# Kernel optimization log

Measured on AMD Instinct MI355X. Metric: run time of the kernel, lower is better.

## Reference

```python
import jax, jax.numpy as jnp
import numpy as np

N, I, R, A, O, HEADS, HW, KS = 16, 128, 256, 256, 256, 8, 24, 3
HC = A // HEADS  # head channels
DN = ('NCHW', 'OIHW', 'NCHW')


def _conv(x, w, padding):
    return jax.lax.conv_general_dilated(x, w, (1, 1), padding, dimension_numbers=DN)


def setup_inputs() -> dict:
    key = jax.random.key(0)
    ks = jax.random.split(key, 16)
    g = lambda k, shape, fan: jax.random.normal(k, shape, jnp.float32) * (fan ** -0.5)
    return {
        'x': jax.random.normal(ks[0], (N, I, HW, HW), jnp.float32),
        'h0': jax.random.normal(ks[1], (N, R, HW, HW), jnp.float32) * 0.1,
        'c0': jax.random.normal(ks[2], (N, R, HW, HW), jnp.float32) * 0.1,
        'w_in': g(ks[3], (R, I, 1, 1), I),
        'b_in': jnp.zeros((R,), jnp.float32),
        'wq_x': g(ks[4], (A, R, KS, KS), R * KS * KS * 2 * HC),
        'wq_h': g(ks[5], (A, R, KS, KS), R * KS * KS * 2 * HC),
        'wk_x': g(ks[6], (A, R, KS, KS), R * KS * KS),
        'wk_h': g(ks[7], (A, R, KS, KS), R * KS * KS),
        'wv_x': g(ks[8], (A, R, KS, KS), R * KS * KS * 2),
        'wv_h': g(ks[9], (A, R, KS, KS), R * KS * KS * 2),
        'bv': jnp.zeros((A,), jnp.float32),
        'wg_a': g(ks[10], (4 * R, A, 1, 1), A * 3),
        'bg': jnp.zeros((4 * R,), jnp.float32),
        'wg_x': g(ks[11], (4 * R, R, KS, KS), R * KS * KS * 3),
        'wg_h': g(ks[12], (4 * R, R, KS, KS), R * KS * KS * 3),
        'w_out': g(ks[13], (O, R, 1, 1), R),
        'b_out': jnp.zeros((O,), jnp.float32),
    }


def reference(x, h0, c0, w_in, b_in, wq_x, wq_h, wk_x, wk_h, wv_x, wv_h, bv,
              wg_a, bg, wg_x, wg_h, w_out, b_out):
    # input accumulation (1x1 conv per input, summed; single input here)
    xin = _conv(x, w_in, 'VALID') + b_in[None, :, None, None]  # [N,R,H,W]
    # q: SAME-padded 3x3 convs of x and h (Accumulate = sum)
    q = _conv(xin, wq_x, 'SAME') + _conv(h0, wq_h, 'SAME')      # [N,A,H,W]
    # k, v: VALID 3x3 convs -> spatially reduced key/value positions
    k = _conv(xin, wk_x, 'VALID') + _conv(h0, wk_h, 'VALID')    # [N,A,H-2,W-2]
    v = _conv(xin, wv_x, 'VALID') + _conv(h0, wv_h, 'VALID') + bv[None, :, None, None]
    Q = HW * HW
    D = (HW - KS + 1) * (HW - KS + 1)
    qh = q.reshape(N, HEADS, HC, Q)
    kh = k.reshape(N, HEADS, HC, D)
    vh = v.reshape(N, HEADS, HC, D)
    w = jax.nn.softmax(jnp.einsum('ngcq,ngcd->ngqd', qh, kh), axis=-1)  # [N,G,Q,D]
    a = jnp.einsum('ngcd,ngqd->ngcq', vh, w).reshape(N, A, HW, HW)
    # fused i,f,g,o gate projections: 1x1 conv on a + 3x3 SAME convs on x and h
    gates = (_conv(a, wg_a, 'VALID') + bg[None, :, None, None]
             + _conv(xin, wg_x, 'SAME') + _conv(h0, wg_h, 'SAME'))      # [N,4R,H,W]
    i, f, gg, o = jnp.split(gates, 4, axis=1)
    c = jax.nn.sigmoid(f) * c0 + jax.nn.sigmoid(i) * jnp.tanh(gg)
    h = jax.nn.sigmoid(o) * jnp.tanh(c)
    return _conv(h, w_out, 'VALID') + b_out[None, :, None, None]
```

## Files before the change

### kernel.cpp

```cpp
#include <hip/hip_runtime.h>
#include <cstddef>

constexpr int kN  = 16;
constexpr int kI  = 128;
constexpr int kHW = 24;
constexpr int kQ  = 576;
constexpr int kD  = 484;
constexpr int kDP = 512;
constexpr int kPP = 676;

constexpr int kKTQKV = 144;
constexpr int kKTG   = 152;
constexpr int kKTO   = 8;

constexpr size_t H_XPAD   = 0;
constexpr size_t H_HPAD   = 2768896;
constexpr size_t H_APQKV  = 5537792;
constexpr size_t H_APG    = 9076736;
constexpr size_t H_APO    = 14057472;
constexpr size_t H_A16    = 14123008;
constexpr size_t H_H16    = 16482304;
constexpr size_t H_Q16C   = 18841600;
constexpr size_t H_KT16   = 21200896;
constexpr size_t H_VC16   = 23298048;

using half8    = __attribute__((ext_vector_type(8))) _Float16;
using floatx16 = __attribute__((ext_vector_type(16))) float;

__device__ __forceinline__ float sigm(float x) { return 1.0f / (1.0f + __expf(-x)); }
__device__ __forceinline__ float tanh_f(float x) {
    float e = __expf(2.0f * fabsf(x));
    float r = 1.0f - 2.0f / (e + 1.0f);
    return copysignf(r, x);
}
__device__ __forceinline__ half8 LD8(const _Float16* p) { return *(const half8*)p; }
__device__ __forceinline__ void ST8(_Float16* p, half8 v) { *(half8*)p = v; }


__global__ void pack_qkv_kernel(const float* __restrict__ wq_x, const float* __restrict__ wq_h,
                                const float* __restrict__ wk_x, const float* __restrict__ wk_h,
                                const float* __restrict__ wv_x, const float* __restrict__ wv_h,
                                _Float16* __restrict__ dst) {
    int pidx = blockIdx.x * 256 + threadIdx.x;
    int j = pidx & 7, row = (pidx >> 3) & 255, hl = (pidx >> 11) & 1, kk = (pidx >> 12) & 1;
    int tile = pidx >> 13;
    int mb = tile / kKTQKV, kt = tile - mb * kKTQKV;
    int k = kt * 32 + kk * 16 + hl * 8 + j;
    int srcs = (k >= 2304) ? 1 : 0;
    int r = k - srcs * 2304;
    int tap = r >> 8, ic = r & 255;
    const float* w;
    if (mb == 0)      w = srcs ? wq_h : wq_x;
    else if (mb == 1) w = srcs ? wk_h : wk_x;
    else              w = srcs ? wv_h : wv_x;
    dst[pidx] = (_Float16)w[((size_t)row * 256 + ic) * 9 + tap];
}

__global__ void pack_gates_kernel(const float* __restrict__ wg_x, const float* __restrict__ wg_h,
                                  const float* __restrict__ wg_a, _Float16* __restrict__ dst) {
    int pidx = blockIdx.x * 256 + threadIdx.x;
    int j = pidx & 7, row = (pidx >> 3) & 255, hl = (pidx >> 11) & 1, kk = (pidx >> 12) & 1;
    int tile = pidx >> 13;
    int mb = tile / kKTG, kt = tile - mb * kKTG;
    int P = mb * 256 + row;
    int T = P >> 5, ch_local = (P >> 2) & 7, g = P & 3;
    int m = g * 256 + T * 8 + ch_local;
    int k = kt * 32 + kk * 16 + hl * 8 + j;
    float val;
    if (k < 4608) {
        int srcs = (k >= 2304) ? 1 : 0;
        int r = k - srcs * 2304;
        int tap = r >> 8, ic = r & 255;
        const float* w = srcs ? wg_h : wg_x;
        val = w[((size_t)m * 256 + ic) * 9 + tap];
    } else {
        val = wg_a[(size_t)m * 256 + (k - 4608)];
    }
    dst[pidx] = (_Float16)val;
}

__global__ void pack_out_kernel(const float* __restrict__ src, _Float16* __restrict__ dst) {
    int pidx = blockIdx.x * 256 + threadIdx.x;
    int j = pidx & 7, row = (pidx >> 3) & 255, hl = (pidx >> 11) & 1, kk = (pidx >> 12) & 1;
    int kt = pidx >> 13;
    int k = kt * 32 + kk * 16 + hl * 8 + j;
    dst[pidx] = (_Float16)src[(size_t)row * 256 + k];
}

__global__ void pad_nhwc_kernel(const float* __restrict__ src, _Float16* __restrict__ dst) {
    __shared__ float tile[32][65];
    int pxt = blockIdx.x, ict = blockIdx.y, n = blockIdx.z;
    int tid = threadIdx.x;
    {
        int icl = tid >> 6, pxl = tid & 63;
        #pragma unroll
        for (int rep = 0; rep < 8; ++rep) {
            int ic = ict * 32 + rep * 4 + icl;
            tile[rep * 4 + icl][pxl] = src[((size_t)n * 256 + ic) * kQ + pxt * 64 + pxl];
        }
    }
    __syncthreads();
    {
        int icl = tid & 31, pxl0 = tid >> 5;
        #pragma unroll
        for (int rep = 0; rep < 8; ++rep) {
            int pxl = rep * 8 + pxl0;
            int px = pxt * 64 + pxl;
            int y = px / kHW, x = px - y * kHW;
            dst[((size_t)n * kPP + (size_t)(y + 1) * 26 + (x + 1)) * 256 + ict * 32 + icl] =
                (_Float16)tile[icl][pxl];
        }
    }
}

__global__ void conv1x1_pad_kernel(const float* __restrict__ x, const float* __restrict__ w,
                                   const float* __restrict__ b, _Float16* __restrict__ out) {
    int px = blockIdx.x * 64 + threadIdx.x;
    int n = blockIdx.z;
    int oc0 = __builtin_amdgcn_readfirstlane(blockIdx.y * 16 + threadIdx.y * 4);
    const float* ip = x + (size_t)n * kI * kQ + px;
    float acc[4] = {0.f, 0.f, 0.f, 0.f};
    #pragma unroll 4
    for (int ic = 0; ic < kI; ++ic) {
        float xv = ip[(size_t)ic * kQ];
        #pragma unroll
        for (int j = 0; j < 4; ++j) acc[j] = fmaf(xv, w[(size_t)(oc0 + j) * kI + ic], acc[j]);
    }
    int y = px / kHW, xc = px - y * kHW;
    _Float16* op = out + ((size_t)n * kPP + (size_t)(y + 1) * 26 + (xc + 1)) * 256 + oc0;
    #pragma unroll
    for (int j = 0; j < 4; ++j) op[j] = (_Float16)(acc[j] + b[oc0 + j]);
}

template<int BMODE, int EMODE>
__global__ __launch_bounds__(256)
void gemm_kernel(const _Float16* __restrict__ Apack,
                 const _Float16* __restrict__ B1, const _Float16* __restrict__ B2,
                 const _Float16* __restrict__ B3,
                 _Float16* __restrict__ q16, _Float16* __restrict__ k16,
                 _Float16* __restrict__ v16, _Float16* __restrict__ h16,
                 const float* __restrict__ c0, float* __restrict__ outf,
                 const float* __restrict__ bias, int Ktiles, int Ktot) {
    __shared__ _Float16 Bs[2][2048];
    const int tid = threadIdx.x;
    const int wv = tid >> 6, lane = tid & 63, l31 = lane & 31, hl = lane >> 5;
    const int nt = blockIdx.x, mb = blockIdx.y, n = blockIdx.z;

    floatx16 acc00 = {}, acc01 = {}, acc10 = {}, acc11 = {};

    const _Float16* aK0 = Apack + (size_t)mb * Ktiles * 8192
                        + hl * 2048 + (size_t)(wv * 64 + l31) * 8;
    const _Float16* aK1 = aK0 + 4096;

    const int px_l = tid >> 2, bc = tid & 3;
    const int px = nt * 64 + px_l;
    const int by = px / kHW, bx = px - by * kHW;
    const int wofs = px_l * 32 + ((bc ^ (px_l & 3)) << 3);
    const int sw = l31 & 3;
    const int r00 = l31 * 32 + ((hl ^ sw) << 3);
    const int r10 = l31 * 32 + (((2 + hl) ^ sw) << 3);

    for (int kt = 0; kt < Ktiles; ++kt) {
        const _Float16* bp;
        if (BMODE == 2 && kt >= 144) {
            bp = B3 + ((size_t)n * kQ + px) * 256 + (kt - 144) * 32 + bc * 8;
        } else if (BMODE == 0 || BMODE == 2) {
            int srcs = (kt >= 72) ? 1 : 0;
            int t2 = kt - srcs * 72;
            int tap = t2 >> 3, ict = t2 & 7;
            int ty = (tap * 11) >> 5;
            int tx = tap - ty * 3;
            const _Float16* img = srcs ? B2 : B1;
            bp = img + ((size_t)n * kPP + (size_t)(by + ty) * 26 + (bx + tx)) * 256
                     + ict * 32 + bc * 8;
        } else {
            bp = B1 + ((size_t)n * kQ + px) * Ktot + kt * 32 + bc * 8;
        }
        half8 bv  = LD8(bp);
        half8 a00 = LD8(aK0);
        half8 a0m = LD8(aK0 + 256);
        half8 a10 = LD8(aK1);
        half8 a1m = LD8(aK1 + 256);
        aK0 += 8192; aK1 += 8192;
        ST8(&Bs[kt & 1][wofs], bv);
        __syncthreads();
        const _Float16* bb = Bs[kt & 1];
        half8 b00 = LD8(bb + r00);
        half8 b01 = LD8(bb + r00 + 1024);
        half8 b10 = LD8(bb + r10);
        half8 b11 = LD8(bb + r10 + 1024);
        acc00 = __builtin_amdgcn_mfma_f32_32x32x16_f16(a00, b00, acc00, 0, 0, 0);
        acc01 = __builtin_amdgcn_mfma_f32_32x32x16_f16(a00, b01, acc01, 0, 0, 0);
        acc10 = __builtin_amdgcn_mfma_f32_32x32x16_f16(a0m, b00, acc10, 0, 0, 0);
        acc11 = __builtin_amdgcn_mfma_f32_32x32x16_f16(a0m, b01, acc11, 0, 0, 0);
        acc00 = __builtin_amdgcn_mfma_f32_32x32x16_f16(a10, b10, acc00, 0, 0, 0);
        acc01 = __builtin_amdgcn_mfma_f32_32x32x16_f16(a10, b11, acc01, 0, 0, 0);
        acc10 = __builtin_amdgcn_mfma_f32_32x32x16_f16(a1m, b10, acc10, 0, 0, 0);
        acc11 = __builtin_amdgcn_mfma_f32_32x32x16_f16(a1m, b11, acc11, 0, 0, 0);
    }

    #pragma unroll
    for (int mtile = 0; mtile < 2; ++mtile) {
        #pragma unroll
        for (int ntile = 0; ntile < 2; ++ntile) {
            const floatx16& A = mtile ? (ntile ? acc11 : acc10) : (ntile ? acc01 : acc00);
            const int pxe = nt * 64 + ntile * 32 + l31;
            if (EMODE == 0) {
                const int mrow = wv * 64 + mtile * 32;
                if (mb == 0) {
                    #pragma unroll
                    for (int r = 0; r < 16; ++r) {
                        int rowi = (r & 3) + 8 * (r >> 2) + 4 * hl;
                        q16[((size_t)n * 256 + mrow + rowi) * kQ + pxe] = (_Float16)A[r];
                    }
                } else {
                    int yy = pxe / kHW, xx = pxe - yy * kHW;
                    if (yy >= 1 && yy <= 22 && xx >= 1 && xx <= 22) {
                        int d = (yy - 1) * 22 + (xx - 1);
                        #pragma unroll
                        for (int r = 0; r < 16; ++r) {
                            int ch = mrow + (r & 3) + 8 * (r >> 2) + 4 * hl;
                            int head = n * 8 + (ch >> 5);
                            if (mb == 1)
                                k16[((size_t)head * kDP + d) * 32 + (ch & 31)] = (_Float16)A[r];
                            else
                                v16[((size_t)head * 32 + (ch & 31)) * kDP + d] =
                                    (_Float16)(A[r] + bias[ch]);
                        }
                    }
                }
            } else if (EMODE == 3) {
                const int T = mb * 8 + wv * 2 + mtile;
                #pragma unroll
                for (int q4 = 0; q4 < 4; ++q4) {
                    int c = T * 8 + 2 * q4 + hl;
                    float iv = A[4 * q4 + 0] + bias[c];
                    float fv = A[4 * q4 + 1] + bias[256 + c];
                    float gv = A[4 * q4 + 2] + bias[512 + c];
                    float ov = A[4 * q4 + 3] + bias[768 + c];
                    float c0v = c0[((size_t)n * 256 + c) * kQ + pxe];
                    float cn = sigm(fv) * c0v + sigm(iv) * tanh_f(gv);
                    h16[((size_t)n * kQ + pxe) * 256 + c] = (_Float16)(sigm(ov) * tanh_f(cn));
                }
            } else {
                const int mrow = wv * 64 + mtile * 32;
                #pragma unroll
                for (int r = 0; r < 16; ++r) {
                    int m = mrow + (r & 3) + 8 * (r >> 2) + 4 * hl;
                    outf[((size_t)n * 256 + m) * kQ + pxe] = A[r] + bias[m];
                }
            }
        }
    }
}

__global__ __launch_bounds__(128)
void attn_kernel(const _Float16* __restrict__ q16c, const _Float16* __restrict__ kT16,
                 const _Float16* __restrict__ vC16, _Float16* __restrict__ a16) {
    const int lane = threadIdx.x & 63;
    const int wv   = threadIdx.x >> 6;
    const int l31 = lane & 31, hl = lane >> 5;
    const int head = blockIdx.y;
    const int n = head >> 3, hd = head & 7;
    const int qt = blockIdx.x * 2 + wv;
    const int q0 = qt * 32;

    half8 qf0, qf1;
    {
        const _Float16* qb = q16c + ((size_t)n * 256 + hd * 32 + hl * 8) * kQ + q0 + l31;
        #pragma unroll
        for (int j = 0; j < 8; ++j) {
            qf0[j] = qb[(size_t)j * kQ];
            qf1[j] = qb[(size_t)(16 + j) * kQ];
        }
    }

    const _Float16* kbase0 = kT16 + ((size_t)head * kDP + l31) * 32 + hl * 8;
    const _Float16* vbase0 = vC16 + ((size_t)head * 32 + l31) * kDP + hl * 8;

    floatx16 acc = {};
    float m_run = -1e30f, l_run = 0.f;

    half8 kf0 = LD8(kbase0);
    half8 kf1 = LD8(kbase0 + 16);

    for (int dt = 0; dt < 16; ++dt) {
        const int d0 = dt * 32;
        floatx16 S = {};
        S = __builtin_amdgcn_mfma_f32_32x32x16_f16(kf0, qf0, S, 0, 0, 0);
        S = __builtin_amdgcn_mfma_f32_32x32x16_f16(kf1, qf1, S, 0, 0, 0);

        half8 vf0 = LD8(vbase0 + d0);
        half8 vf1 = LD8(vbase0 + d0 + 16);
        if (dt < 15) {
            kf0 = LD8(kbase0 + (size_t)(d0 + 32) * 32);
            kf1 = LD8(kbase0 + (size_t)(d0 + 32) * 32 + 16);
        }

        if (dt == 15) {
            #pragma unroll
            for (int r = 0; r < 16; ++r)
                if (!(hl == 0 && r < 4)) S[r] = -1e30f;
        }

        float tmax = S[0];
        #pragma unroll
        for (int r = 1; r < 16; ++r) tmax = fmaxf(tmax, S[r]);
        tmax = fmaxf(tmax, __shfl_xor(tmax, 32));
        float mnew = fmaxf(m_run, tmax);
        float f = __expf(m_run - mnew);
        float p[16], psum = 0.f;
        #pragma unroll
        for (int r = 0; r < 16; ++r) { p[r] = __expf(S[r] - mnew); psum += p[r]; }
        psum += __shfl_xor(psum, 32);
        l_run = f * l_run + psum;
        #pragma unroll
        for (int r = 0; r < 16; ++r) acc[r] *= f;
        m_run = mnew;

        float other[16];
        #pragma unroll
        for (int r = 0; r < 16; ++r) other[r] = __shfl_xor(p[r], 32);
        half8 pf0, pf1;
        #pragma unroll
        for (int t = 0; t < 4; ++t) {
            pf0[t]     = (_Float16)(hl ? other[4 + t]  : p[t]);
            pf0[4 + t] = (_Float16)(hl ? p[4 + t]      : other[t]);
            pf1[t]     = (_Float16)(hl ? other[12 + t] : p[8 + t]);
            pf1[4 + t] = (_Float16)(hl ? p[12 + t]     : other[8 + t]);
        }

        acc = __builtin_amdgcn_mfma_f32_32x32x16_f16(vf0, pf0, acc, 0, 0, 0);
        acc = __builtin_amdgcn_mfma_f32_32x32x16_f16(vf1, pf1, acc, 0, 0, 0);
    }

    float inv = 1.f / l_run;
    _Float16* ap = a16 + ((size_t)n * kQ + q0 + l31) * 256 + hd * 32;
    #pragma unroll
    for (int r = 0; r < 16; ++r) {
        int c = (r & 3) + 8 * (r >> 2) + 4 * hl;
        ap[c] = (_Float16)(acc[r] * inv);
    }
}

extern "C" void kernel_launch(void* const* d_in, const int* in_sizes, int n_in,
                              void* d_out, int out_size, void* d_ws, size_t ws_size,
                              hipStream_t stream) {
    (void)in_sizes; (void)n_in; (void)out_size; (void)ws_size;
    const float* x     = (const float*)d_in[0];
    const float* h0    = (const float*)d_in[1];
    const float* c0    = (const float*)d_in[2];
    const float* w_in  = (const float*)d_in[3];
    const float* b_in  = (const float*)d_in[4];
    const float* wq_x  = (const float*)d_in[5];
    const float* wq_h  = (const float*)d_in[6];
    const float* wk_x  = (const float*)d_in[7];
    const float* wk_h  = (const float*)d_in[8];
    const float* wv_x  = (const float*)d_in[9];
    const float* wv_h  = (const float*)d_in[10];
    const float* bv    = (const float*)d_in[11];
    const float* wg_a  = (const float*)d_in[12];
    const float* bg    = (const float*)d_in[13];
    const float* wg_x  = (const float*)d_in[14];
    const float* wg_h  = (const float*)d_in[15];
    const float* w_out = (const float*)d_in[16];
    const float* b_out = (const float*)d_in[17];

    _Float16* wh = (_Float16*)d_ws;
    _Float16* xpad16  = wh + H_XPAD;
    _Float16* hpad16  = wh + H_HPAD;
    _Float16* apqkv   = wh + H_APQKV;
    _Float16* apg     = wh + H_APG;
    _Float16* apo     = wh + H_APO;
    _Float16* a16     = wh + H_A16;
    _Float16* h16     = wh + H_H16;
    _Float16* q16c    = wh + H_Q16C;
    _Float16* kT16    = wh + H_KT16;
    _Float16* vC16    = wh + H_VC16;

    hipMemsetAsync(wh, 0, 11075584, stream);

    pack_qkv_kernel<<<13824, 256, 0, stream>>>(wq_x, wq_h, wk_x, wk_h, wv_x, wv_h, apqkv);
    pack_gates_kernel<<<19456, 256, 0, stream>>>(wg_x, wg_h, wg_a, apg);
    pack_out_kernel<<<256, 256, 0, stream>>>(w_out, apo);

    pad_nhwc_kernel<<<dim3(9, 8, kN), 256, 0, stream>>>(h0, hpad16);
    conv1x1_pad_kernel<<<dim3(9, 16, kN), dim3(64, 4), 0, stream>>>(x, w_in, b_in, xpad16);

    gemm_kernel<0, 0><<<dim3(9, 3, kN), 256, 0, stream>>>(
        apqkv, xpad16, hpad16, nullptr, q16c, kT16, vC16, nullptr,
        nullptr, nullptr, bv, kKTQKV, 0);

    attn_kernel<<<dim3(9, 128), 128, 0, stream>>>(q16c, kT16, vC16, a16);

    gemm_kernel<2, 3><<<dim3(9, 4, kN), 256, 0, stream>>>(
        apg, xpad16, hpad16, a16, nullptr, nullptr, nullptr, h16,
        c0, nullptr, bg, kKTG, 0);

    gemm_kernel<1, 2><<<dim3(9, 1, kN), 256, 0, stream>>>(
        apo, h16, nullptr, nullptr, nullptr, nullptr, nullptr, nullptr,
        nullptr, (float*)d_out, b_out, kKTO, 256);
}
```

Baseline: 526.2 us.

## Halve GEMM M-tile to 128 rows and pad LDS rows instead of XOR swizzle

The GEMM block tile shrinks from 256x64 to 128x64, so each wave now computes one 32-row M-tile with two accumulators instead of four. The grid doubles along M, and the weight pack kernels are reorganised to a 128-row tile layout. The LDS B tile now uses a padded row stride of 40 halves in place of the XOR swizzle, and a second barrier is added per K step. The intent is to launch more blocks for better occupancy and CU coverage. The cost is halved A/B reuse per block, twice as many B loads from global memory, and extra synchronisation.

```diff
diff --git a/kernel.cpp b/kernel.cpp
--- a/kernel.cpp
+++ b/kernel.cpp
@@ -42,27 +42,28 @@
                                 const float* __restrict__ wv_x, const float* __restrict__ wv_h,
                                 _Float16* __restrict__ dst) {
     int pidx = blockIdx.x * 256 + threadIdx.x;
-    int j = pidx & 7, row = (pidx >> 3) & 255, hl = (pidx >> 11) & 1, kk = (pidx >> 12) & 1;
-    int tile = pidx >> 13;
-    int mb = tile / kKTQKV, kt = tile - mb * kKTQKV;
+    int j = pidx & 7, row = (pidx >> 3) & 127, hl = (pidx >> 10) & 1, kk = (pidx >> 11) & 1;
+    int tile = pidx >> 12;
+    int mt = tile / kKTQKV, kt = tile - mt * kKTQKV;
+    int m = mt * 128 + row;
     int k = kt * 32 + kk * 16 + hl * 8 + j;
     int srcs = (k >= 2304) ? 1 : 0;
     int r = k - srcs * 2304;
     int tap = r >> 8, ic = r & 255;
-    const float* w;
-    if (mb == 0)      w = srcs ? wq_h : wq_x;
-    else if (mb == 1) w = srcs ? wk_h : wk_x;
-    else              w = srcs ? wv_h : wv_x;
-    dst[pidx] = (_Float16)w[((size_t)row * 256 + ic) * 9 + tap];
+    const float* w; int mm;
+    if (m < 256)      { w = srcs ? wq_h : wq_x; mm = m; }
+    else if (m < 512) { w = srcs ? wk_h : wk_x; mm = m - 256; }
+    else              { w = srcs ? wv_h : wv_x; mm = m - 512; }
+    dst[pidx] = (_Float16)w[((size_t)mm * 256 + ic) * 9 + tap];
 }
 
 __global__ void pack_gates_kernel(const float* __restrict__ wg_x, const float* __restrict__ wg_h,
                                   const float* __restrict__ wg_a, _Float16* __restrict__ dst) {
     int pidx = blockIdx.x * 256 + threadIdx.x;
-    int j = pidx & 7, row = (pidx >> 3) & 255, hl = (pidx >> 11) & 1, kk = (pidx >> 12) & 1;
-    int tile = pidx >> 13;
-    int mb = tile / kKTG, kt = tile - mb * kKTG;
-    int P = mb * 256 + row;
+    int j = pidx & 7, row = (pidx >> 3) & 127, hl = (pidx >> 10) & 1, kk = (pidx >> 11) & 1;
+    int tile = pidx >> 12;
+    int mt = tile / kKTG, kt = tile - mt * kKTG;
+    int P = mt * 128 + row;
     int T = P >> 5, ch_local = (P >> 2) & 7, g = P & 3;
     int m = g * 256 + T * 8 + ch_local;
     int k = kt * 32 + kk * 16 + hl * 8 + j;
@@ -81,10 +82,12 @@
 
 __global__ void pack_out_kernel(const float* __restrict__ src, _Float16* __restrict__ dst) {
     int pidx = blockIdx.x * 256 + threadIdx.x;
-    int j = pidx & 7, row = (pidx >> 3) & 255, hl = (pidx >> 11) & 1, kk = (pidx >> 12) & 1;
-    int kt = pidx >> 13;
+    int j = pidx & 7, row = (pidx >> 3) & 127, hl = (pidx >> 10) & 1, kk = (pidx >> 11) & 1;
+    int tile = pidx >> 12;
+    int mt = tile >> 3, kt = tile & 7;
+    int m = mt * 128 + row;
     int k = kt * 32 + kk * 16 + hl * 8 + j;
-    dst[pidx] = (_Float16)src[(size_t)row * 256 + k];
+    dst[pidx] = (_Float16)src[(size_t)m * 256 + k];
 }
 
 __global__ void pad_nhwc_kernel(const float* __restrict__ src, _Float16* __restrict__ dst) {
@@ -141,24 +144,21 @@
                  _Float16* __restrict__ v16, _Float16* __restrict__ h16,
                  const float* __restrict__ c0, float* __restrict__ outf,
                  const float* __restrict__ bias, int Ktiles, int Ktot) {
-    __shared__ _Float16 Bs[2][2048];
+    __shared__ _Float16 Bs[2][2560];
     const int tid = threadIdx.x;
     const int wv = tid >> 6, lane = tid & 63, l31 = lane & 31, hl = lane >> 5;
-    const int nt = blockIdx.x, mb = blockIdx.y, n = blockIdx.z;
-
-    floatx16 acc00 = {}, acc01 = {}, acc10 = {}, acc11 = {};
-
-    const _Float16* aK0 = Apack + (size_t)mb * Ktiles * 8192
-                        + hl * 2048 + (size_t)(wv * 64 + l31) * 8;
-    const _Float16* aK1 = aK0 + 4096;
+    const int nt = blockIdx.x, mt = blockIdx.y, n = blockIdx.z;
+
+    floatx16 acc0 = {}, acc1 = {};
+
+    const _Float16* aptr = Apack + (size_t)mt * Ktiles * 4096
+                         + (size_t)hl * 1024 + (size_t)(wv * 32 + l31) * 8;
 
     const int px_l = tid >> 2, bc = tid & 3;
     const int px = nt * 64 + px_l;
     const int by = px / kHW, bx = px - by * kHW;
-    const int wofs = px_l * 32 + ((bc ^ (px_l & 3)) << 3);
-    const int sw = l31 & 3;
-    const int r00 = l31 * 32 + ((hl ^ sw) << 3);
-    const int r10 = l31 * 32 + (((2 + hl) ^ sw) << 3);
+    const int wofs = px_l * 40 + bc * 8;
+    const int r0 = l31 * 40 + hl * 8;
 
     for (int kt = 0; kt < Ktiles; ++kt) {
         const _Float16* bp;
@@ -176,79 +176,71 @@
         } else {
             bp = B1 + ((size_t)n * kQ + px) * Ktot + kt * 32 + bc * 8;
         }
-        half8 bv  = LD8(bp);
-        half8 a00 = LD8(aK0);
-        half8 a0m = LD8(aK0 + 256);
-        half8 a10 = LD8(aK1);
-        half8 a1m = LD8(aK1 + 256);
-        aK0 += 8192; aK1 += 8192;
+        half8 bv = LD8(bp);
+        half8 a0 = LD8(aptr);
+        half8 a1 = LD8(aptr + 2048);
+        aptr += 4096;
         ST8(&Bs[kt & 1][wofs], bv);
         __syncthreads();
         const _Float16* bb = Bs[kt & 1];
-        half8 b00 = LD8(bb + r00);
-        half8 b01 = LD8(bb + r00 + 1024);
-        half8 b10 = LD8(bb + r10);
-        half8 b11 = LD8(bb + r10 + 1024);
-        acc00 = __builtin_amdgcn_mfma_f32_32x32x16_f16(a00, b00, acc00, 0, 0, 0);
-        acc01 = __builtin_amdgcn_mfma_f32_32x32x16_f16(a00, b01, acc01, 0, 0, 0);
-        acc10 = __builtin_amdgcn_mfma_f32_32x32x16_f16(a0m, b00, acc10, 0, 0, 0);
-        acc11 = __builtin_amdgcn_mfma_f32_32x32x16_f16(a0m, b01, acc11, 0, 0, 0);
-        acc00 = __builtin_amdgcn_mfma_f32_32x32x16_f16(a10, b10, acc00, 0, 0, 0);
-        acc01 = __builtin_amdgcn_mfma_f32_32x32x16_f16(a10, b11, acc01, 0, 0, 0);
-        acc10 = __builtin_amdgcn_mfma_f32_32x32x16_f16(a1m, b10, acc10, 0, 0, 0);
-        acc11 = __builtin_amdgcn_mfma_f32_32x32x16_f16(a1m, b11, acc11, 0, 0, 0);
+        half8 b00 = LD8(bb + r0);
+        half8 b01 = LD8(bb + r0 + 1280);
+        half8 b10 = LD8(bb + r0 + 16);
+        half8 b11 = LD8(bb + r0 + 1296);
+        acc0 = __builtin_amdgcn_mfma_f32_32x32x16_f16(a0, b00, acc0, 0, 0, 0);
+        acc1 = __builtin_amdgcn_mfma_f32_32x32x16_f16(a0, b01, acc1, 0, 0, 0);
+        acc0 = __builtin_amdgcn_mfma_f32_32x32x16_f16(a1, b10, acc0, 0, 0, 0);
+        acc1 = __builtin_amdgcn_mfma_f32_32x32x16_f16(a1, b11, acc1, 0, 0, 0);
+        __syncthreads();
     }
 
     #pragma unroll
-    for (int mtile = 0; mtile < 2; ++mtile) {
-        #pragma unroll
-        for (int ntile = 0; ntile < 2; ++ntile) {
-            const floatx16& A = mtile ? (ntile ? acc11 : acc10) : (ntile ? acc01 : acc00);
-            const int pxe = nt * 64 + ntile * 32 + l31;
-            if (EMODE == 0) {
-                const int mrow = wv * 64 + mtile * 32;
-                if (mb == 0) {
+    for (int ntile = 0; ntile < 2; ++ntile) {
+        const floatx16& A = ntile ? acc1 : acc0;
+        const int pxe = nt * 64 + ntile * 32 + l31;
+        if (EMODE == 0) {
+            const int mrow = mt * 128 + wv * 32;
+            if (mrow < 256) {
+                #pragma unroll
+                for (int r = 0; r < 16; ++r) {
+                    int rowi = (r & 3) + 8 * (r >> 2) + 4 * hl;
+                    q16[((size_t)n * 256 + mrow + rowi) * kQ + pxe] = (_Float16)A[r];
+                }
+            } else {
+                int yy = pxe / kHW, xx = pxe - yy * kHW;
+                if (yy >= 1 && yy <= 22 && xx >= 1 && xx <= 22) {
+                    int d = (yy - 1) * 22 + (xx - 1);
                     #pragma unroll
                     for (int r = 0; r < 16; ++r) {
-                        int rowi = (r & 3) + 8 * (r >> 2) + 4 * hl;
-                        q16[((size_t)n * 256 + mrow + rowi) * kQ + pxe] = (_Float16)A[r];
-                    }
-                } else {
-                    int yy = pxe / kHW, xx = pxe - yy * kHW;
-                    if (yy >= 1 && yy <= 22 && xx >= 1 && xx <= 22) {
-                        int d = (yy - 1) * 22 + (xx - 1);
-                        #pragma unroll
-                        for (int r = 0; r < 16; ++r) {
-                            int ch = mrow + (r & 3) + 8 * (r >> 2) + 4 * hl;
-                            int head = n * 8 + (ch >> 5);
-                            if (mb == 1)
-                                k16[((size_t)head * kDP + d) * 32 + (ch & 31)] = (_Float16)A[r];
-                            else
-                                v16[((size_t)head * 32 + (ch & 31)) * kDP + d] =
-                                    (_Float16)(A[r] + bias[ch]);
-                        }
+                        int ch = (mrow & 255) + (r & 3) + 8 * (r >> 2) + 4 * hl;
+                        int head = n * 8 + (ch >> 5);
+                        if (mrow < 512)
+                            k16[((size_t)head * kDP + d) * 32 + (ch & 31)] = (_Float16)A[r];
+                        else
+                            v16[((size_t)head * 32 + (ch & 31)) * kDP + d] =
+                                (_Float16)(A[r] + bias[ch]);
                     }
                 }
-            } else if (EMODE == 3) {
-                const int T = mb * 8 + wv * 2 + mtile;
-                #pragma unroll
-                for (int q4 = 0; q4 < 4; ++q4) {
-                    int c = T * 8 + 2 * q4 + hl;
-                    float iv = A[4 * q4 + 0] + bias[c];
-                    float fv = A[4 * q4 + 1] + bias[256 + c];
-                    float gv = A[4 * q4 + 2] + bias[512 + c];
-                    float ov = A[4 * q4 + 3] + bias[768 + c];
-                    float c0v = c0[((size_t)n * 256 + c) * kQ + pxe];
-                    float cn = sigm(fv) * c0v + sigm(iv) * tanh_f(gv);
-                    h16[((size_t)n * kQ + pxe) * 256 + c] = (_Float16)(sigm(ov) * tanh_f(cn));
-                }
-            } else {
-                const int mrow = wv * 64 + mtile * 32;
-                #pragma unroll
-                for (int r = 0; r < 16; ++r) {
-                    int m = mrow + (r & 3) + 8 * (r >> 2) + 4 * hl;
-                    outf[((size_t)n * 256 + m) * kQ + pxe] = A[r] + bias[m];
-                }
+            }
+        } else if (EMODE == 3) {
+            const int T = mt * 4 + wv;
+            #pragma unroll
+            for (int q4 = 0; q4 < 4; ++q4) {
+                int c = T * 8 + 2 * q4 + hl;
+                float iv = A[4 * q4 + 0] + bias[c];
+                float fv = A[4 * q4 + 1] + bias[256 + c];
+                float gv = A[4 * q4 + 2] + bias[512 + c];
+                float ov = A[4 * q4 + 3] + bias[768 + c];
+                float c0v = c0[((size_t)n * 256 + c) * kQ + pxe];
+                float cn = sigm(fv) * c0v + sigm(iv) * tanh_f(gv);
+                h16[((size_t)n * kQ + pxe) * 256 + c] = (_Float16)(sigm(ov) * tanh_f(cn));
+            }
+        } else {
+            const int mrow = mt * 128 + wv * 32;
+            #pragma unroll
+            for (int r = 0; r < 16; ++r) {
+                int m = mrow + (r & 3) + 8 * (r >> 2) + 4 * hl;
+                outf[((size_t)n * 256 + m) * kQ + pxe] = A[r] + bias[m];
             }
         }
     }
@@ -387,17 +379,17 @@
     pad_nhwc_kernel<<<dim3(9, 8, kN), 256, 0, stream>>>(h0, hpad16);
     conv1x1_pad_kernel<<<dim3(9, 16, kN), dim3(64, 4), 0, stream>>>(x, w_in, b_in, xpad16);
 
-    gemm_kernel<0, 0><<<dim3(9, 3, kN), 256, 0, stream>>>(
+    gemm_kernel<0, 0><<<dim3(9, 6, kN), 256, 0, stream>>>(
         apqkv, xpad16, hpad16, nullptr, q16c, kT16, vC16, nullptr,
         nullptr, nullptr, bv, kKTQKV, 0);
 
     attn_kernel<<<dim3(9, 128), 128, 0, stream>>>(q16c, kT16, vC16, a16);
 
-    gemm_kernel<2, 3><<<dim3(9, 4, kN), 256, 0, stream>>>(
+    gemm_kernel<2, 3><<<dim3(9, 8, kN), 256, 0, stream>>>(
         apg, xpad16, hpad16, a16, nullptr, nullptr, nullptr, h16,
         c0, nullptr, bg, kKTG, 0);
 
-    gemm_kernel<1, 2><<<dim3(9, 1, kN), 256, 0, stream>>>(
+    gemm_kernel<1, 2><<<dim3(9, 2, kN), 256, 0, stream>>>(
         apo, h16, nullptr, nullptr, nullptr, nullptr, nullptr, nullptr,
         nullptr, (float*)d_out, b_out, kKTO, 256);
 }
```

New measurement: 509.9 us. -3.1%, faster.

## Software-pipeline GEMM main loop with two-deep register prefetch and padded LDS

Applied to the files above, without the earlier changes.

Restructures the MFMA GEMM K-loop into a manually unrolled two-stage pipeline. A and B fragments for tile kt+2 and kt+3 are loaded into registers while the current tiles are computed, so global load latency is hidden behind MFMAs. The XOR-swizzled shared layout is replaced by a row stride of 40 halves to avoid bank conflicts, and the fragment offsets are adjusted to match. This costs extra registers for the prefetched fragments and assumes Ktiles is even. The variable mb is also renamed to mt.

```diff
diff --git a/kernel.cpp b/kernel.cpp
--- a/kernel.cpp
+++ b/kernel.cpp
@@ -44,14 +44,14 @@
     int pidx = blockIdx.x * 256 + threadIdx.x;
     int j = pidx & 7, row = (pidx >> 3) & 255, hl = (pidx >> 11) & 1, kk = (pidx >> 12) & 1;
     int tile = pidx >> 13;
-    int mb = tile / kKTQKV, kt = tile - mb * kKTQKV;
+    int mt = tile / kKTQKV, kt = tile - mt * kKTQKV;
     int k = kt * 32 + kk * 16 + hl * 8 + j;
     int srcs = (k >= 2304) ? 1 : 0;
     int r = k - srcs * 2304;
     int tap = r >> 8, ic = r & 255;
     const float* w;
-    if (mb == 0)      w = srcs ? wq_h : wq_x;
-    else if (mb == 1) w = srcs ? wk_h : wk_x;
+    if (mt == 0)      w = srcs ? wq_h : wq_x;
+    else if (mt == 1) w = srcs ? wk_h : wk_x;
     else              w = srcs ? wv_h : wv_x;
     dst[pidx] = (_Float16)w[((size_t)row * 256 + ic) * 9 + tap];
 }
@@ -61,8 +61,8 @@
     int pidx = blockIdx.x * 256 + threadIdx.x;
     int j = pidx & 7, row = (pidx >> 3) & 255, hl = (pidx >> 11) & 1, kk = (pidx >> 12) & 1;
     int tile = pidx >> 13;
-    int mb = tile / kKTG, kt = tile - mb * kKTG;
-    int P = mb * 256 + row;
+    int mt = tile / kKTG, kt = tile - mt * kKTG;
+    int P = mt * 256 + row;
     int T = P >> 5, ch_local = (P >> 2) & 7, g = P & 3;
     int m = g * 256 + T * 8 + ch_local;
     int k = kt * 32 + kk * 16 + hl * 8 + j;
@@ -141,62 +141,103 @@
                  _Float16* __restrict__ v16, _Float16* __restrict__ h16,
                  const float* __restrict__ c0, float* __restrict__ outf,
                  const float* __restrict__ bias, int Ktiles, int Ktot) {
-    __shared__ _Float16 Bs[2][2048];
+    __shared__ _Float16 Bs[2][2560];
     const int tid = threadIdx.x;
     const int wv = tid >> 6, lane = tid & 63, l31 = lane & 31, hl = lane >> 5;
-    const int nt = blockIdx.x, mb = blockIdx.y, n = blockIdx.z;
+    const int nt = blockIdx.x, mt = blockIdx.y, n = blockIdx.z;
 
     floatx16 acc00 = {}, acc01 = {}, acc10 = {}, acc11 = {};
 
-    const _Float16* aK0 = Apack + (size_t)mb * Ktiles * 8192
-                        + hl * 2048 + (size_t)(wv * 64 + l31) * 8;
-    const _Float16* aK1 = aK0 + 4096;
+    const _Float16* abase = Apack + (size_t)mt * Ktiles * 8192
+                          + hl * 2048 + (size_t)(wv * 64 + l31) * 8;
 
     const int px_l = tid >> 2, bc = tid & 3;
     const int px = nt * 64 + px_l;
     const int by = px / kHW, bx = px - by * kHW;
-    const int wofs = px_l * 32 + ((bc ^ (px_l & 3)) << 3);
-    const int sw = l31 & 3;
-    const int r00 = l31 * 32 + ((hl ^ sw) << 3);
-    const int r10 = l31 * 32 + (((2 + hl) ^ sw) << 3);
-
-    for (int kt = 0; kt < Ktiles; ++kt) {
-        const _Float16* bp;
-        if (BMODE == 2 && kt >= 144) {
-            bp = B3 + ((size_t)n * kQ + px) * 256 + (kt - 144) * 32 + bc * 8;
-        } else if (BMODE == 0 || BMODE == 2) {
+    const int wofs = px_l * 40 + bc * 8;
+    const int r0 = l31 * 40 + hl * 8;
+
+    auto bptr = [&](int kt) -> const _Float16* {
+        if (BMODE == 2 && kt >= 144)
+            return B3 + ((size_t)n * kQ + px) * 256 + (kt - 144) * 32 + bc * 8;
+        if (BMODE == 0 || BMODE == 2) {
             int srcs = (kt >= 72) ? 1 : 0;
             int t2 = kt - srcs * 72;
             int tap = t2 >> 3, ict = t2 & 7;
             int ty = (tap * 11) >> 5;
             int tx = tap - ty * 3;
             const _Float16* img = srcs ? B2 : B1;
-            bp = img + ((size_t)n * kPP + (size_t)(by + ty) * 26 + (bx + tx)) * 256
-                     + ict * 32 + bc * 8;
-        } else {
-            bp = B1 + ((size_t)n * kQ + px) * Ktot + kt * 32 + bc * 8;
-        }
-        half8 bv  = LD8(bp);
-        half8 a00 = LD8(aK0);
-        half8 a0m = LD8(aK0 + 256);
-        half8 a10 = LD8(aK1);
-        half8 a1m = LD8(aK1 + 256);
-        aK0 += 8192; aK1 += 8192;
-        ST8(&Bs[kt & 1][wofs], bv);
-        __syncthreads();
-        const _Float16* bb = Bs[kt & 1];
-        half8 b00 = LD8(bb + r00);
-        half8 b01 = LD8(bb + r00 + 1024);
-        half8 b10 = LD8(bb + r10);
-        half8 b11 = LD8(bb + r10 + 1024);
-        acc00 = __builtin_amdgcn_mfma_f32_32x32x16_f16(a00, b00, acc00, 0, 0, 0);
-        acc01 = __builtin_amdgcn_mfma_f32_32x32x16_f16(a00, b01, acc01, 0, 0, 0);
-        acc10 = __builtin_amdgcn_mfma_f32_32x32x16_f16(a0m, b00, acc10, 0, 0, 0);
-        acc11 = __builtin_amdgcn_mfma_f32_32x32x16_f16(a0m, b01, acc11, 0, 0, 0);
-        acc00 = __builtin_amdgcn_mfma_f32_32x32x16_f16(a10, b10, acc00, 0, 0, 0);
-        acc01 = __builtin_amdgcn_mfma_f32_32x32x16_f16(a10, b11, acc01, 0, 0, 0);
-        acc10 = __builtin_amdgcn_mfma_f32_32x32x16_f16(a1m, b10, acc10, 0, 0, 0);
-        acc11 = __builtin_amdgcn_mfma_f32_32x32x16_f16(a1m, b11, acc11, 0, 0, 0);
+            return img + ((size_t)n * kPP + (size_t)(by + ty) * 26 + (bx + tx)) * 256
+                       + ict * 32 + bc * 8;
+        }
+        return B1 + ((size_t)n * kQ + px) * Ktot + kt * 32 + bc * 8;
+    };
+
+    half8 bq0, bq1;
+    half8 aq0[4], aq1[4];
+
+    bq0 = LD8(bptr(0));
+    bq1 = LD8(bptr(1));
+    {
+        const _Float16* ap = abase;
+        aq0[0] = LD8(ap);            aq0[1] = LD8(ap + 256);
+        aq0[2] = LD8(ap + 4096);     aq0[3] = LD8(ap + 4096 + 256);
+        ap = abase + 8192;
+        aq1[0] = LD8(ap);            aq1[1] = LD8(ap + 256);
+        aq1[2] = LD8(ap + 4096);     aq1[3] = LD8(ap + 4096 + 256);
+    }
+    ST8(&Bs[0][wofs], bq0);
+    __syncthreads();
+
+    for (int kt = 0; kt < Ktiles; kt += 2) {
+        {
+            const _Float16* bb = Bs[0];
+            half8 b00 = LD8(bb + r0);
+            half8 b01 = LD8(bb + r0 + 1280);
+            half8 b10 = LD8(bb + r0 + 16);
+            half8 b11 = LD8(bb + r0 + 1296);
+            half8 a00 = aq0[0], a01 = aq0[1], a10 = aq0[2], a11 = aq0[3];
+            if (kt + 2 < Ktiles) {
+                bq0 = LD8(bptr(kt + 2));
+                const _Float16* ap = abase + (size_t)(kt + 2) * 8192;
+                aq0[0] = LD8(ap);          aq0[1] = LD8(ap + 256);
+                aq0[2] = LD8(ap + 4096);   aq0[3] = LD8(ap + 4096 + 256);
+            }
+            acc00 = __builtin_amdgcn_mfma_f32_32x32x16_f16(a00, b00, acc00, 0, 0, 0);
+            acc01 = __builtin_amdgcn_mfma_f32_32x32x16_f16(a00, b01, acc01, 0, 0, 0);
+            acc10 = __builtin_amdgcn_mfma_f32_32x32x16_f16(a01, b00, acc10, 0, 0, 0);
+            acc11 = __builtin_amdgcn_mfma_f32_32x32x16_f16(a01, b01, acc11, 0, 0, 0);
+            acc00 = __builtin_amdgcn_mfma_f32_32x32x16_f16(a10, b10, acc00, 0, 0, 0);
+            acc01 = __builtin_amdgcn_mfma_f32_32x32x16_f16(a10, b11, acc01, 0, 0, 0);
+            acc10 = __builtin_amdgcn_mfma_f32_32x32x16_f16(a11, b10, acc10, 0, 0, 0);
+            acc11 = __builtin_amdgcn_mfma_f32_32x32x16_f16(a11, b11, acc11, 0, 0, 0);
+            ST8(&Bs[1][wofs], bq1);
+            __syncthreads();
+        }
+        {
+            const _Float16* bb = Bs[1];
+            half8 b00 = LD8(bb + r0);
+            half8 b01 = LD8(bb + r0 + 1280);
+            half8 b10 = LD8(bb + r0 + 16);
+            half8 b11 = LD8(bb + r0 + 1296);
+            half8 a00 = aq1[0], a01 = aq1[1], a10 = aq1[2], a11 = aq1[3];
+            if (kt + 3 < Ktiles) {
+                bq1 = LD8(bptr(kt + 3));
+                const _Float16* ap = abase + (size_t)(kt + 3) * 8192;
+                aq1[0] = LD8(ap);          aq1[1] = LD8(ap + 256);
+                aq1[2] = LD8(ap + 4096);   aq1[3] = LD8(ap + 4096 + 256);
+            }
+            acc00 = __builtin_amdgcn_mfma_f32_32x32x16_f16(a00, b00, acc00, 0, 0, 0);
+            acc01 = __builtin_amdgcn_mfma_f32_32x32x16_f16(a00, b01, acc01, 0, 0, 0);
+            acc10 = __builtin_amdgcn_mfma_f32_32x32x16_f16(a01, b00, acc10, 0, 0, 0);
+            acc11 = __builtin_amdgcn_mfma_f32_32x32x16_f16(a01, b01, acc11, 0, 0, 0);
+            acc00 = __builtin_amdgcn_mfma_f32_32x32x16_f16(a10, b10, acc00, 0, 0, 0);
+            acc01 = __builtin_amdgcn_mfma_f32_32x32x16_f16(a10, b11, acc01, 0, 0, 0);
+            acc10 = __builtin_amdgcn_mfma_f32_32x32x16_f16(a11, b10, acc10, 0, 0, 0);
+            acc11 = __builtin_amdgcn_mfma_f32_32x32x16_f16(a11, b11, acc11, 0, 0, 0);
+            if (kt + 2 < Ktiles) ST8(&Bs[0][wofs], bq0);
+            __syncthreads();
+        }
     }
 
     #pragma unroll
@@ -207,7 +248,7 @@
             const int pxe = nt * 64 + ntile * 32 + l31;
             if (EMODE == 0) {
                 const int mrow = wv * 64 + mtile * 32;
-                if (mb == 0) {
+                if (mt == 0) {
                     #pragma unroll
                     for (int r = 0; r < 16; ++r) {
                         int rowi = (r & 3) + 8 * (r >> 2) + 4 * hl;
@@ -221,7 +262,7 @@
                         for (int r = 0; r < 16; ++r) {
                             int ch = mrow + (r & 3) + 8 * (r >> 2) + 4 * hl;
                             int head = n * 8 + (ch >> 5);
-                            if (mb == 1)
+                            if (mt == 1)
                                 k16[((size_t)head * kDP + d) * 32 + (ch & 31)] = (_Float16)A[r];
                             else
                                 v16[((size_t)head * 32 + (ch & 31)) * kDP + d] =
@@ -230,7 +271,7 @@
                     }
                 }
             } else if (EMODE == 3) {
-                const int T = mb * 8 + wv * 2 + mtile;
+                const int T = mt * 8 + wv * 2 + mtile;
                 #pragma unroll
                 for (int q4 = 0; q4 < 4; ++q4) {
                     int c = T * 8 + 2 * q4 + hl;
```

New measurement: 485.9 us. -7.7%, faster.
